# Kernel tuning notes

Measured on AMD Instinct MI355X. Metric: run time of the kernel, lower is better.

Reference implementation:

```python
import jax, jax.numpy as jnp
import numpy as np

N = 4096          # batch size; must equal COV_DIM because of the triangular mask
INPUT_DIM = 2048
COV_DIM = 4096
OUTPUT_DIM = 1


def _glorot(key, shape):
    fan_in = shape[0] if len(shape) > 1 else shape[0]
    fan_out = shape[-1]
    std = np.sqrt(2.0 / (fan_in + fan_out))
    return jax.random.normal(key, shape, dtype=jnp.float32) * std


def setup_inputs() -> dict:
    key = jax.random.key(0)
    ks = jax.random.split(key, 8)
    return {
        "x": jax.random.normal(ks[0], (N, INPUT_DIM), dtype=jnp.float32),
        "mu_kernel": _glorot(ks[1], (INPUT_DIM, OUTPUT_DIM)),
        "mu_bias": _glorot(ks[2], (OUTPUT_DIM,)),
        "cov_kernel": _glorot(ks[3], (INPUT_DIM, COV_DIM)),
        "cov_bias": _glorot(ks[4], (COV_DIM,)),
        "var_kernel": _glorot(ks[5], (INPUT_DIM, OUTPUT_DIM)),
        "var_bias": _glorot(ks[6], (OUTPUT_DIM,)),
        "rho_kernel": _glorot(ks[7], (2 * COV_DIM,)),
    }


def reference(x, mu_kernel, mu_bias, cov_kernel, cov_bias, var_kernel, var_bias, rho_kernel):
    n = x.shape[0]
    cov_dim = cov_kernel.shape[1]

    # mean head
    output_mu = x @ mu_kernel + mu_bias                      # (n, 1)

    # low-rank covariance features
    c = x @ cov_kernel + cov_bias                            # (n, cov_dim)

    # diagonal variances: softplus + eps, squeezed to (n,)
    d = jnp.squeeze(jnp.log1p(jnp.exp(x @ var_kernel + var_bias)) + 1e-8, axis=-1)

    # rho[i, j] = sum_k c[i, k] * w_a[k] + sum_k c[j, k] * w_b[k]
    # (equivalent to tiling a=(n,n,cov_dim), b=(n,n,cov_dim), concat, dot with rho_kernel
    #  -- but without materializing the O(n^2 * cov_dim) intermediate)
    u = c @ rho_kernel[:cov_dim]                             # (n,)
    v = c @ rho_kernel[cov_dim:]                             # (n,)
    rho = u[:, None] + v[None, :]                            # (n, n)

    # lower-triangular mask (tfp.math.fill_triangular of ones)
    rho = rho * jnp.tril(jnp.ones((n, n), dtype=x.dtype))

    # L @ L.T
    mm = rho @ rho.T                                         # (n, n)

    # scatter diagonal (tf.linalg.set_diag)
    i = jnp.arange(n)
    output_cov = mm.at[i, i].set(d)

    return output_mu, output_cov
```

## Files before the change

kernel.cpp:

```cpp
#include <hip/hip_runtime.h>
#include <math.h>

#define N_ROWS 4096
#define K_DIM  2048
#define C_DIM  4096

__device__ __forceinline__ float4 ld4(const float* p) {
    return *reinterpret_cast<const float4*>(p);
}

template<int NV>
__device__ __forceinline__ void block_reduce(float* vals, float (*lds)[8]) {
    int lane = threadIdx.x & 63;
    int wv   = threadIdx.x >> 6;
#pragma unroll
    for (int i = 0; i < NV; ++i) {
        float val = vals[i];
#pragma unroll
        for (int off = 32; off > 0; off >>= 1)
            val += __shfl_down(val, off, 64);
        if (lane == 0) lds[i][wv] = val;
    }
    __syncthreads();
    if (threadIdx.x == 0) {
        int nw = blockDim.x >> 6;
#pragma unroll
        for (int i = 0; i < NV; ++i) {
            float s = 0.f;
            for (int w = 0; w < nw; ++w) s += lds[i][w];
            vals[i] = s;
        }
    }
}

__global__ __launch_bounds__(256) void k_proj(const float* __restrict__ covk,
                                              const float* __restrict__ covb,
                                              const float* __restrict__ rho,
                                              float* __restrict__ pa,
                                              float* __restrict__ pb,
                                              float* __restrict__ cab) {
    __shared__ float lds[2][8];
    int row = blockIdx.x;
    const float* src = (row < K_DIM) ? covk + (size_t)row * C_DIM : covb;
    const float* wa = rho;
    const float* wb = rho + C_DIM;
    float s[2] = {0.f, 0.f};
    int t = threadIdx.x;
#pragma unroll
    for (int it = 0; it < 4; ++it) {
        int j = (it * 256 + t) * 4;
        float4 c = ld4(src + j);
        float4 a = ld4(wa + j);
        float4 b = ld4(wb + j);
        s[0] += c.x * a.x + c.y * a.y + c.z * a.z + c.w * a.w;
        s[1] += c.x * b.x + c.y * b.y + c.z * b.z + c.w * b.w;
    }
    block_reduce<2>(s, lds);
    if (t == 0) {
        if (row < K_DIM) { pa[row] = s[0]; pb[row] = s[1]; }
        else             { cab[0] = s[0]; cab[1] = s[1]; }
    }
}

__global__ __launch_bounds__(256) void k_xdots(const float* __restrict__ x,
                                               const float* __restrict__ pa,
                                               const float* __restrict__ pb,
                                               const float* __restrict__ muk,
                                               const float* __restrict__ vark,
                                               const float* __restrict__ cab,
                                               const float* __restrict__ mub,
                                               const float* __restrict__ varb,
                                               float* __restrict__ u,
                                               float* __restrict__ v,
                                               float* __restrict__ dd,
                                               float* __restrict__ out_mu) {
    __shared__ float lds[4][8];
    int i = blockIdx.x;
    const float* xr = x + (size_t)i * K_DIM;
    float s[4] = {0.f, 0.f, 0.f, 0.f};
    int t = threadIdx.x;
#pragma unroll
    for (int it = 0; it < 2; ++it) {
        int j = (it * 256 + t) * 4;
        float4 xv = ld4(xr + j);
        float4 a  = ld4(pa + j);
        float4 b  = ld4(pb + j);
        float4 m  = ld4(muk + j);
        float4 w  = ld4(vark + j);
        s[0] += xv.x * a.x + xv.y * a.y + xv.z * a.z + xv.w * a.w;
        s[1] += xv.x * b.x + xv.y * b.y + xv.z * b.z + xv.w * b.w;
        s[2] += xv.x * m.x + xv.y * m.y + xv.z * m.z + xv.w * m.w;
        s[3] += xv.x * w.x + xv.y * w.y + xv.z * w.z + xv.w * w.w;
    }
    block_reduce<4>(s, lds);
    if (t == 0) {
        u[i] = s[0] + cab[0];
        v[i] = s[1] + cab[1];
        out_mu[i] = s[2] + mub[0];
        float tt = s[3] + varb[0];
        float sp = (tt > 20.f) ? tt : log1pf(expf(tt));
        dd[i] = sp + 1e-8f;
    }
}

__global__ __launch_bounds__(1024) void k_scan(const float* __restrict__ v,
                                               float* __restrict__ S1,
                                               float* __restrict__ S2) {
    __shared__ float l1[1024];
    __shared__ float l2[1024];
    int t = threadIdx.x;
    float4 vv = ld4(v + t * 4);
    float a0 = vv.x;
    float a1 = a0 + vv.y;
    float a2 = a1 + vv.z;
    float a3 = a2 + vv.w;
    float q0 = vv.x * vv.x;
    float q1 = q0 + vv.y * vv.y;
    float q2 = q1 + vv.z * vv.z;
    float q3 = q2 + vv.w * vv.w;
    l1[t] = a3;
    l2[t] = q3;
    __syncthreads();
    for (int off = 1; off < 1024; off <<= 1) {
        float x1 = (t >= off) ? l1[t - off] : 0.f;
        float x2 = (t >= off) ? l2[t - off] : 0.f;
        __syncthreads();
        l1[t] += x1;
        l2[t] += x2;
        __syncthreads();
    }
    float base1 = (t > 0) ? l1[t - 1] : 0.f;
    float base2 = (t > 0) ? l2[t - 1] : 0.f;
    float4 o1 = make_float4(base1 + a0, base1 + a1, base1 + a2, base1 + a3);
    float4 o2 = make_float4(base2 + q0, base2 + q1, base2 + q2, base2 + q3);
    *reinterpret_cast<float4*>(S1 + t * 4) = o1;
    *reinterpret_cast<float4*>(S2 + t * 4) = o2;
}

__global__ __launch_bounds__(256) void k_cov(const float* __restrict__ u,
                                             const float* __restrict__ S1,
                                             const float* __restrict__ S2,
                                             const float* __restrict__ dd,
                                             float* __restrict__ out) {
    int i  = blockIdx.y;
    int j0 = (blockIdx.x * 256 + threadIdx.x) * 4;
    float ui = u[i];
    float4 uj = ld4(u + j0);
    float4 r;
    if (j0 + 3 < i) {
        float4 s1 = ld4(S1 + j0);
        float4 s2 = ld4(S2 + j0);
        r.x = (float)(j0 + 1) * ui * uj.x + (ui + uj.x) * s1.x + s2.x;
        r.y = (float)(j0 + 2) * ui * uj.y + (ui + uj.y) * s1.y + s2.y;
        r.z = (float)(j0 + 3) * ui * uj.z + (ui + uj.z) * s1.z + s2.z;
        r.w = (float)(j0 + 4) * ui * uj.w + (ui + uj.w) * s1.w + s2.w;
    } else if (j0 > i) {
        float mi = (float)(i + 1);
        float s1i = S1[i], s2i = S2[i];
        r.x = mi * ui * uj.x + (ui + uj.x) * s1i + s2i;
        r.y = mi * ui * uj.y + (ui + uj.y) * s1i + s2i;
        r.z = mi * ui * uj.z + (ui + uj.z) * s1i + s2i;
        r.w = mi * ui * uj.w + (ui + uj.w) * s1i + s2i;
    } else {
        float s1i = S1[i], s2i = S2[i];
        float di = dd[i];
        float uu[4] = {uj.x, uj.y, uj.z, uj.w};
        float rr[4];
#pragma unroll
        for (int e = 0; e < 4; ++e) {
            int j = j0 + e;
            if (j < i)
                rr[e] = (float)(j + 1) * ui * uu[e] + (ui + uu[e]) * S1[j] + S2[j];
            else if (j == i)
                rr[e] = di;
            else
                rr[e] = (float)(i + 1) * ui * uu[e] + (ui + uu[e]) * s1i + s2i;
        }
        r = make_float4(rr[0], rr[1], rr[2], rr[3]);
    }
    *reinterpret_cast<float4*>(out + (size_t)i * C_DIM + j0) = r;
}

extern "C" void kernel_launch(void* const* d_in, const int* in_sizes, int n_in,
                              void* d_out, int out_size, void* d_ws, size_t ws_size,
                              hipStream_t stream) {
    const float* x    = (const float*)d_in[0];
    const float* muk  = (const float*)d_in[1];
    const float* mub  = (const float*)d_in[2];
    const float* covk = (const float*)d_in[3];
    const float* covb = (const float*)d_in[4];
    const float* vark = (const float*)d_in[5];
    const float* varb = (const float*)d_in[6];
    const float* rho  = (const float*)d_in[7];

    float* out_mu  = (float*)d_out;
    float* out_cov = (float*)d_out + N_ROWS;

    float* ws  = (float*)d_ws;
    float* pa  = ws;
    float* pb  = pa + K_DIM;
    float* cab = pb + K_DIM;
    float* u   = cab + 64;
    float* v   = u + C_DIM;
    float* dd  = v + C_DIM;
    float* S1  = dd + C_DIM;
    float* S2  = S1 + C_DIM;

    hipLaunchKernelGGL(k_proj, dim3(K_DIM + 1), dim3(256), 0, stream,
                       covk, covb, rho, pa, pb, cab);
    hipLaunchKernelGGL(k_xdots, dim3(N_ROWS), dim3(256), 0, stream,
                       x, pa, pb, muk, vark, cab, mub, varb, u, v, dd, out_mu);
    hipLaunchKernelGGL(k_scan, dim3(1), dim3(1024), 0, stream, v, S1, S2);
    hipLaunchKernelGGL(k_cov, dim3(C_DIM / 1024, N_ROWS), dim3(256), 0, stream,
                       u, S1, S2, dd, out_cov);
}
```

Measured before the change: 135.6 us.

## Use wave-per-row reductions and fuse prefix scan into covariance kernel

The projection and x-dot kernels now assign one 64-lane wavefront per row and reduce with shuffles only, removing the LDS block reduction and the __syncthreads barrier. The single-block scan kernel is removed: each covariance block recomputes the prefix sums of v and v^2 into LDS, then writes four output rows using those LDS values. This drops one launch and the serial single-block scan, at the cost of repeating the 4096-element scan in each of 1024 blocks.

Result: slower. 139.2 us (+2.7%).

```diff
diff --git a/kernel.cpp b/kernel.cpp
--- a/kernel.cpp
+++ b/kernel.cpp
@@ -7,30 +7,6 @@
 
 __device__ __forceinline__ float4 ld4(const float* p) {
     return *reinterpret_cast<const float4*>(p);
-}
-
-template<int NV>
-__device__ __forceinline__ void block_reduce(float* vals, float (*lds)[8]) {
-    int lane = threadIdx.x & 63;
-    int wv   = threadIdx.x >> 6;
-#pragma unroll
-    for (int i = 0; i < NV; ++i) {
-        float val = vals[i];
-#pragma unroll
-        for (int off = 32; off > 0; off >>= 1)
-            val += __shfl_down(val, off, 64);
-        if (lane == 0) lds[i][wv] = val;
-    }
-    __syncthreads();
-    if (threadIdx.x == 0) {
-        int nw = blockDim.x >> 6;
-#pragma unroll
-        for (int i = 0; i < NV; ++i) {
-            float s = 0.f;
-            for (int w = 0; w < nw; ++w) s += lds[i][w];
-            vals[i] = s;
-        }
-    }
 }
 
 __global__ __launch_bounds__(256) void k_proj(const float* __restrict__ covk,
@@ -39,26 +15,30 @@
                                               float* __restrict__ pa,
                                               float* __restrict__ pb,
                                               float* __restrict__ cab) {
-    __shared__ float lds[2][8];
-    int row = blockIdx.x;
-    const float* src = (row < K_DIM) ? covk + (size_t)row * C_DIM : covb;
+    const int w    = (blockIdx.x * 256 + threadIdx.x) >> 6;
+    const int lane = threadIdx.x & 63;
+    if (w > K_DIM) return;
+    const float* src = (w < K_DIM) ? covk + (size_t)w * C_DIM : covb;
     const float* wa = rho;
     const float* wb = rho + C_DIM;
-    float s[2] = {0.f, 0.f};
-    int t = threadIdx.x;
-#pragma unroll
-    for (int it = 0; it < 4; ++it) {
-        int j = (it * 256 + t) * 4;
+    float sa = 0.f, sb = 0.f;
+#pragma unroll 4
+    for (int it = 0; it < 16; ++it) {
+        const int j = (it * 64 + lane) * 4;
         float4 c = ld4(src + j);
         float4 a = ld4(wa + j);
         float4 b = ld4(wb + j);
-        s[0] += c.x * a.x + c.y * a.y + c.z * a.z + c.w * a.w;
-        s[1] += c.x * b.x + c.y * b.y + c.z * b.z + c.w * b.w;
-    }
-    block_reduce<2>(s, lds);
-    if (t == 0) {
-        if (row < K_DIM) { pa[row] = s[0]; pb[row] = s[1]; }
-        else             { cab[0] = s[0]; cab[1] = s[1]; }
+        sa += c.x * a.x + c.y * a.y + c.z * a.z + c.w * a.w;
+        sb += c.x * b.x + c.y * b.y + c.z * b.z + c.w * b.w;
+    }
+#pragma unroll
+    for (int off = 32; off > 0; off >>= 1) {
+        sa += __shfl_down(sa, off, 64);
+        sb += __shfl_down(sb, off, 64);
+    }
+    if (lane == 0) {
+        if (w < K_DIM) { pa[w] = sa; pb[w] = sb; }
+        else           { cab[0] = sa; cab[1] = sb; }
     }
 }
 
@@ -74,111 +54,124 @@
                                                float* __restrict__ v,
                                                float* __restrict__ dd,
                                                float* __restrict__ out_mu) {
-    __shared__ float lds[4][8];
-    int i = blockIdx.x;
+    const int i    = (blockIdx.x * 256 + threadIdx.x) >> 6;
+    const int lane = threadIdx.x & 63;
     const float* xr = x + (size_t)i * K_DIM;
-    float s[4] = {0.f, 0.f, 0.f, 0.f};
-    int t = threadIdx.x;
-#pragma unroll
-    for (int it = 0; it < 2; ++it) {
-        int j = (it * 256 + t) * 4;
+    float s0 = 0.f, s1 = 0.f, s2 = 0.f, s3 = 0.f;
+#pragma unroll 2
+    for (int it = 0; it < 8; ++it) {
+        const int j = (it * 64 + lane) * 4;
         float4 xv = ld4(xr + j);
         float4 a  = ld4(pa + j);
         float4 b  = ld4(pb + j);
         float4 m  = ld4(muk + j);
-        float4 w  = ld4(vark + j);
-        s[0] += xv.x * a.x + xv.y * a.y + xv.z * a.z + xv.w * a.w;
-        s[1] += xv.x * b.x + xv.y * b.y + xv.z * b.z + xv.w * b.w;
-        s[2] += xv.x * m.x + xv.y * m.y + xv.z * m.z + xv.w * m.w;
-        s[3] += xv.x * w.x + xv.y * w.y + xv.z * w.z + xv.w * w.w;
-    }
-    block_reduce<4>(s, lds);
-    if (t == 0) {
-        u[i] = s[0] + cab[0];
-        v[i] = s[1] + cab[1];
-        out_mu[i] = s[2] + mub[0];
-        float tt = s[3] + varb[0];
+        float4 wv = ld4(vark + j);
+        s0 += xv.x * a.x + xv.y * a.y + xv.z * a.z + xv.w * a.w;
+        s1 += xv.x * b.x + xv.y * b.y + xv.z * b.z + xv.w * b.w;
+        s2 += xv.x * m.x + xv.y * m.y + xv.z * m.z + xv.w * m.w;
+        s3 += xv.x * wv.x + xv.y * wv.y + xv.z * wv.z + xv.w * wv.w;
+    }
+#pragma unroll
+    for (int off = 32; off > 0; off >>= 1) {
+        s0 += __shfl_down(s0, off, 64);
+        s1 += __shfl_down(s1, off, 64);
+        s2 += __shfl_down(s2, off, 64);
+        s3 += __shfl_down(s3, off, 64);
+    }
+    if (lane == 0) {
+        u[i] = s0 + cab[0];
+        v[i] = s1 + cab[1];
+        out_mu[i] = s2 + mub[0];
+        float tt = s3 + varb[0];
         float sp = (tt > 20.f) ? tt : log1pf(expf(tt));
         dd[i] = sp + 1e-8f;
     }
 }
 
-__global__ __launch_bounds__(1024) void k_scan(const float* __restrict__ v,
-                                               float* __restrict__ S1,
-                                               float* __restrict__ S2) {
-    __shared__ float l1[1024];
-    __shared__ float l2[1024];
-    int t = threadIdx.x;
-    float4 vv = ld4(v + t * 4);
-    float a0 = vv.x;
-    float a1 = a0 + vv.y;
-    float a2 = a1 + vv.z;
-    float a3 = a2 + vv.w;
-    float q0 = vv.x * vv.x;
-    float q1 = q0 + vv.y * vv.y;
-    float q2 = q1 + vv.z * vv.z;
-    float q3 = q2 + vv.w * vv.w;
-    l1[t] = a3;
-    l2[t] = q3;
+__global__ __launch_bounds__(256, 4) void k_cov(const float* __restrict__ u,
+                                                const float* __restrict__ v,
+                                                const float* __restrict__ dd,
+                                                float* __restrict__ out) {
+    __shared__ float sS1[C_DIM];
+    __shared__ float sS2[C_DIM];
+    __shared__ float tmp[2][256];
+    const int t = threadIdx.x;
+
+    float ve[16], p1[16], p2[16];
+#pragma unroll
+    for (int g = 0; g < 4; ++g) {
+        float4 w = ld4(v + t * 16 + g * 4);
+        ve[g * 4 + 0] = w.x; ve[g * 4 + 1] = w.y;
+        ve[g * 4 + 2] = w.z; ve[g * 4 + 3] = w.w;
+    }
+    float r1 = 0.f, r2 = 0.f;
+#pragma unroll
+    for (int e = 0; e < 16; ++e) {
+        r1 += ve[e];         p1[e] = r1;
+        r2 += ve[e] * ve[e]; p2[e] = r2;
+    }
+    tmp[0][t] = r1; tmp[1][t] = r2;
     __syncthreads();
-    for (int off = 1; off < 1024; off <<= 1) {
-        float x1 = (t >= off) ? l1[t - off] : 0.f;
-        float x2 = (t >= off) ? l2[t - off] : 0.f;
+    for (int off = 1; off < 256; off <<= 1) {
+        float a1 = (t >= off) ? tmp[0][t - off] : 0.f;
+        float a2 = (t >= off) ? tmp[1][t - off] : 0.f;
         __syncthreads();
-        l1[t] += x1;
-        l2[t] += x2;
+        tmp[0][t] += a1; tmp[1][t] += a2;
         __syncthreads();
     }
-    float base1 = (t > 0) ? l1[t - 1] : 0.f;
-    float base2 = (t > 0) ? l2[t - 1] : 0.f;
-    float4 o1 = make_float4(base1 + a0, base1 + a1, base1 + a2, base1 + a3);
-    float4 o2 = make_float4(base2 + q0, base2 + q1, base2 + q2, base2 + q3);
-    *reinterpret_cast<float4*>(S1 + t * 4) = o1;
-    *reinterpret_cast<float4*>(S2 + t * 4) = o2;
-}
-
-__global__ __launch_bounds__(256) void k_cov(const float* __restrict__ u,
-                                             const float* __restrict__ S1,
-                                             const float* __restrict__ S2,
-                                             const float* __restrict__ dd,
-                                             float* __restrict__ out) {
-    int i  = blockIdx.y;
-    int j0 = (blockIdx.x * 256 + threadIdx.x) * 4;
-    float ui = u[i];
-    float4 uj = ld4(u + j0);
-    float4 r;
-    if (j0 + 3 < i) {
-        float4 s1 = ld4(S1 + j0);
-        float4 s2 = ld4(S2 + j0);
-        r.x = (float)(j0 + 1) * ui * uj.x + (ui + uj.x) * s1.x + s2.x;
-        r.y = (float)(j0 + 2) * ui * uj.y + (ui + uj.y) * s1.y + s2.y;
-        r.z = (float)(j0 + 3) * ui * uj.z + (ui + uj.z) * s1.z + s2.z;
-        r.w = (float)(j0 + 4) * ui * uj.w + (ui + uj.w) * s1.w + s2.w;
-    } else if (j0 > i) {
-        float mi = (float)(i + 1);
-        float s1i = S1[i], s2i = S2[i];
-        r.x = mi * ui * uj.x + (ui + uj.x) * s1i + s2i;
-        r.y = mi * ui * uj.y + (ui + uj.y) * s1i + s2i;
-        r.z = mi * ui * uj.z + (ui + uj.z) * s1i + s2i;
-        r.w = mi * ui * uj.w + (ui + uj.w) * s1i + s2i;
-    } else {
-        float s1i = S1[i], s2i = S2[i];
-        float di = dd[i];
-        float uu[4] = {uj.x, uj.y, uj.z, uj.w};
-        float rr[4];
-#pragma unroll
-        for (int e = 0; e < 4; ++e) {
-            int j = j0 + e;
-            if (j < i)
-                rr[e] = (float)(j + 1) * ui * uu[e] + (ui + uu[e]) * S1[j] + S2[j];
-            else if (j == i)
-                rr[e] = di;
-            else
-                rr[e] = (float)(i + 1) * ui * uu[e] + (ui + uu[e]) * s1i + s2i;
+    const float b1 = (t > 0) ? tmp[0][t - 1] : 0.f;
+    const float b2 = (t > 0) ? tmp[1][t - 1] : 0.f;
+#pragma unroll
+    for (int e = 0; e < 16; ++e) {
+        sS1[t * 16 + e] = b1 + p1[e];
+        sS2[t * 16 + e] = b2 + p2[e];
+    }
+    __syncthreads();
+
+    const int i0 = blockIdx.x * 4;
+    for (int r = 0; r < 4; ++r) {
+        const int i = i0 + r;
+        const float ui  = u[i];
+        const float s1i = sS1[i];
+        const float s2i = sS2[i];
+        float* orow = out + ((size_t)i << 12);
+#pragma unroll
+        for (int c = 0; c < 4; ++c) {
+            const int j0 = (c * 256 + t) * 4;
+            float4 uj = ld4(u + j0);
+            float4 rr;
+            if (j0 + 3 < i) {
+                float4 s1 = *reinterpret_cast<const float4*>(sS1 + j0);
+                float4 s2 = *reinterpret_cast<const float4*>(sS2 + j0);
+                rr.x = (float)(j0 + 1) * ui * uj.x + (ui + uj.x) * s1.x + s2.x;
+                rr.y = (float)(j0 + 2) * ui * uj.y + (ui + uj.y) * s1.y + s2.y;
+                rr.z = (float)(j0 + 3) * ui * uj.z + (ui + uj.z) * s1.z + s2.z;
+                rr.w = (float)(j0 + 4) * ui * uj.w + (ui + uj.w) * s1.w + s2.w;
+            } else if (j0 > i) {
+                const float mi = (float)(i + 1);
+                rr.x = mi * ui * uj.x + (ui + uj.x) * s1i + s2i;
+                rr.y = mi * ui * uj.y + (ui + uj.y) * s1i + s2i;
+                rr.z = mi * ui * uj.z + (ui + uj.z) * s1i + s2i;
+                rr.w = mi * ui * uj.w + (ui + uj.w) * s1i + s2i;
+            } else {
+                const float di = dd[i];
+                float uu[4] = {uj.x, uj.y, uj.z, uj.w};
+                float re[4];
+#pragma unroll
+                for (int e = 0; e < 4; ++e) {
+                    const int j = j0 + e;
+                    if (j < i)
+                        re[e] = (float)(j + 1) * ui * uu[e] + (ui + uu[e]) * sS1[j] + sS2[j];
+                    else if (j == i)
+                        re[e] = di;
+                    else
+                        re[e] = (float)(i + 1) * ui * uu[e] + (ui + uu[e]) * s1i + s2i;
+                }
+                rr = make_float4(re[0], re[1], re[2], re[3]);
+            }
+            *reinterpret_cast<float4*>(orow + j0) = rr;
         }
-        r = make_float4(rr[0], rr[1], rr[2], rr[3]);
-    }
-    *reinterpret_cast<float4*>(out + (size_t)i * C_DIM + j0) = r;
+    }
 }
 
 extern "C" void kernel_launch(void* const* d_in, const int* in_sizes, int n_in,
@@ -203,14 +196,11 @@
     float* u   = cab + 64;
     float* v   = u + C_DIM;
     float* dd  = v + C_DIM;
-    float* S1  = dd + C_DIM;
-    float* S2  = S1 + C_DIM;
-
-    hipLaunchKernelGGL(k_proj, dim3(K_DIM + 1), dim3(256), 0, stream,
+
+    hipLaunchKernelGGL(k_proj, dim3(513), dim3(256), 0, stream,
                        covk, covb, rho, pa, pb, cab);
-    hipLaunchKernelGGL(k_xdots, dim3(N_ROWS), dim3(256), 0, stream,
+    hipLaunchKernelGGL(k_xdots, dim3(1024), dim3(256), 0, stream,
                        x, pa, pb, muk, vark, cab, mub, varb, u, v, dd, out_mu);
-    hipLaunchKernelGGL(k_scan, dim3(1), dim3(1024), 0, stream, v, S1, S2);
-    hipLaunchKernelGGL(k_cov, dim3(C_DIM / 1024, N_ROWS), dim3(256), 0, stream,
-                       u, S1, S2, dd, out_cov);
-}
+    hipLaunchKernelGGL(k_cov, dim3(1024), dim3(256), 0, stream,
+                       u, v, dd, out_cov);
+}
```
